# Kernel optimization log

Hardware: AMD Instinct MI355X
Metric: run time of the kernel (lower is better)

## Reference

```python
import jax, jax.numpy as jnp
import numpy as np

N_ENTITY = 30000
N_MOVIE = 6000
D = 384            # entity_hidden_size = hidden_size // 2
H = 768            # hidden_size
HT = 768           # token_hidden_size
N_LAYER = 12
N_BLOCK = 2
N_HEAD = 12
HEAD_DIM = H // N_HEAD
NUM_REL = 12
NUM_BASES = 8
E_KG = 200000
E_C = 200000
E_S = 80000
B = 16
LE = 48
LT = 256


def setup_inputs() -> dict:
    key = jax.random.key(0)
    ks = iter(jax.random.split(key, 48))
    nk = lambda: next(ks)
    rn = lambda shape, s=0.02: jax.random.normal(nk(), shape, dtype=jnp.float32) * s
    ri = lambda shape, m: jax.random.randint(nk(), shape, 0, m)
    return {
        'node_embeds': rn((N_ENTITY, D), 0.05),
        'rgcn_bases': rn((NUM_BASES, D, D)),
        'rgcn_comp': rn((NUM_REL, NUM_BASES), 0.3),
        'rgcn_root': rn((D, D)),
        'rgcn_bias': rn((D,), 0.01),
        'ep1_w1': rn((D, D // 2)), 'ep1_b1': rn((D // 2,), 0.01),
        'ep1_w2': rn((D // 2, D)), 'ep1_b2': rn((D,), 0.01),
        'ep2_w': rn((D, H)), 'ep2_b': rn((H,), 0.01),
        'tp1_w1': rn((HT, HT // 2)), 'tp1_b1': rn((HT // 2,), 0.01),
        'tp1_w2': rn((HT // 2, HT)), 'tp1_b2': rn((HT,), 0.01),
        'tp2_w': rn((HT, H)), 'tp2_b': rn((H,), 0.01),
        'ca_w': rn((H, H)),
        'pp1_w1': rn((H, H // 2)), 'pp1_b1': rn((H // 2,), 0.01),
        'pp1_w2': rn((H // 2, H)), 'pp1_b2': rn((H,), 0.01),
        'pp2_w': rn((H, N_LAYER * N_BLOCK * H)), 'pp2_b': rn((N_LAYER * N_BLOCK * H,), 0.01),
        'token_embeds': jax.random.normal(nk(), (B, LT, HT), dtype=jnp.float32),
        'edge_index': ri((2, E_KG), N_ENTITY),
        'edge_type': ri((E_KG,), NUM_REL),
        'edge_index_c': ri((2, E_C), N_ENTITY),
        'edge_index_t_s': ri((2, E_S), N_MOVIE),
        'edge_index_i_s': ri((2, E_S), N_MOVIE),
        'movie_to_entity': ri((N_MOVIE,), N_ENTITY),
        'entity_ids': ri((B, LE), N_ENTITY),
    }


def _mlp(x, w1, b1, w2, b2):
    return jax.nn.relu(x @ w1 + b1) @ w2 + b2


def _gcn(x, edge_index):
    # CustomGCNConv: add self loops, symmetric deg^{-1/2} norm, scatter-add
    n = x.shape[0]
    loop = jnp.arange(n)
    src = jnp.concatenate([edge_index[0], loop])
    dst = jnp.concatenate([edge_index[1], loop])
    deg = jax.ops.segment_sum(jnp.ones_like(dst, dtype=x.dtype), dst, num_segments=n)
    dis = deg ** -0.5  # deg >= 1 due to self loops
    norm = dis[src] * dis[dst]
    return jax.ops.segment_sum(norm[:, None] * x[src], dst, num_segments=n)


def _rgcn(x, edge_index, edge_type, bases, comp, root, bias):
    # PyG RGCNConv with basis decomposition, mean aggregation per relation
    n = x.shape[0]
    src, dst = edge_index[0], edge_index[1]
    W = jnp.einsum('rb,bio->rio', comp, bases)  # [R, D, D]
    out = x @ root + bias
    for r in range(NUM_REL):
        mask = (edge_type == r).astype(x.dtype)
        cnt = jax.ops.segment_sum(mask, dst, num_segments=n)
        norm = mask / jnp.maximum(cnt[dst], 1.0)
        h = x @ W[r]
        out = out + jax.ops.segment_sum(norm[:, None] * h[src], dst, num_segments=n)
    return out


def reference(node_embeds, rgcn_bases, rgcn_comp, rgcn_root, rgcn_bias,
              ep1_w1, ep1_b1, ep1_w2, ep1_b2, ep2_w, ep2_b,
              tp1_w1, tp1_b1, tp1_w2, tp1_b2, tp2_w, tp2_b,
              ca_w, pp1_w1, pp1_b1, pp1_w2, pp1_b2, pp2_w, pp2_b,
              token_embeds, edge_index, edge_type, edge_index_c,
              edge_index_t_s, edge_index_i_s, movie_to_entity, entity_ids):
    # ---- get_entity_embeds ----
    ent0 = _rgcn(node_embeds, edge_index, edge_type, rgcn_bases, rgcn_comp, rgcn_root, rgcn_bias) + node_embeds
    nf = ent0[movie_to_entity]  # sorted_indices == idx_to_id_tensor (keys are range(n_movie))
    ts1 = _gcn(nf, edge_index_t_s)
    ts2 = _gcn(ts1, edge_index_t_s)  # ts3 computed in original but unused -> skipped
    mt = (ts1 + ts2) * 0.5
    is1 = _gcn(nf, edge_index_i_s)
    is2 = _gcn(is1, edge_index_i_s)
    mi = (is1 + is2) * 0.5
    mm = (mt + mi) * 0.5
    c1 = _gcn(ent0, edge_index_c)
    c2 = _gcn(c1, edge_index_c)
    c3 = _gcn(c2, edge_index_c)
    ent = (c1 + c2 + c3 + ent0) * 0.25
    ent = ent.at[movie_to_entity].add(mm)  # index_add_
    ent = _mlp(ent, ep1_w1, ep1_b1, ep1_w2, ep1_b2) + ent
    ent = ent @ ep2_w + ep2_b  # [N_ENTITY, H]
    # ---- forward ----
    eemb = ent[entity_ids]  # [B, LE, H]
    tok = _mlp(token_embeds, tp1_w1, tp1_b1, tp1_w2, tp1_b2) + token_embeds
    tok = tok @ tp2_w + tp2_b  # [B, LT, H]
    attn = jnp.einsum('bth,beh->bte', tok @ ca_w, eemb) / H
    w = jax.nn.softmax(attn, axis=2)  # output_entity=False branch
    prompt = jnp.einsum('bte,beh->bth', w, eemb) + tok
    prompt = _mlp(prompt, pp1_w1, pp1_b1, pp1_w2, pp1_b2) + prompt
    prompt = prompt @ pp2_w + pp2_b  # [B, LT, N_LAYER*N_BLOCK*H]
    prompt = prompt.reshape(B, LT, N_LAYER, N_BLOCK, N_HEAD, HEAD_DIM)
    return prompt.transpose(2, 3, 0, 4, 1, 5)  # [n_layer, n_block, B, n_head, LT, head_dim]
```

## Files before the change

### kernel.cpp

```cpp
#include <hip/hip_runtime.h>
#include <hip/hip_bf16.h>
#include <cstdint>
#include <cstddef>


namespace {

constexpr int NE   = 30000;
constexpr int NM   = 6000;
constexpr int Dm   = 384;
constexpr int Hm   = 768;
constexpr int EKG  = 200000;
constexpr int EC   = 200000;
constexpr int ES   = 80000;
constexpr int Bc   = 16;
constexpr int LE   = 48;
constexpr int NTOK = 4096;
constexpr int NO   = 18432;

constexpr size_t NBf = (size_t)NE * Dm;
constexpr size_t MBF = (size_t)NM * Dm;

constexpr size_t P_XB    = 0;
constexpr size_t P_WCT   = 5760000;
constexpr size_t P_CNT   = 6644736;
constexpr size_t P_ENT0  = 7004736;
constexpr size_t P_HH    = 18524736;
constexpr size_t P_DIS   = 53084736;
constexpr size_t P_E0B   = 0;
constexpr size_t P_C1B   = 2880000;
constexpr size_t P_C2B   = 5760000;
constexpr size_t P_NFB   = 8640000;
constexpr size_t P_T1B   = 9800000;
constexpr size_t P_G1    = 11000000;
constexpr size_t P_ACC   = 41564736;
constexpr size_t P_ENTB  = 55600000;
constexpr size_t P_HIDB  = 0;
constexpr size_t P_ENT2B = 2880000;
constexpr size_t P_E768B = 8640000;
constexpr size_t P_TOKB  = 20160000;
constexpr size_t P_THIDB = 21732864;
constexpr size_t P_TOK1B = 22519296;
constexpr size_t P_TOK2B = 24092160;
constexpr size_t P_QB    = 25665024;
constexpr size_t P_EEMB  = 27237888;
constexpr size_t P_PR0   = 27532800;
constexpr size_t P_PR0B  = 30678528;
constexpr size_t P_PHIDB = 32251392;
constexpr size_t P_WT    = 74000000;
constexpr size_t S_ROOT  = 0;
constexpr size_t S_EP1A  = 147456;
constexpr size_t S_EP1B  = 221184;
constexpr size_t S_EP2   = 294912;
constexpr size_t S_TP1A  = 589824;
constexpr size_t S_TP1B  = 884736;
constexpr size_t S_TP2   = 1179648;
constexpr size_t S_CAW   = 1769472;
constexpr size_t S_PP1A  = 2359296;
constexpr size_t S_PP1B  = 2654208;

constexpr size_t WI       = 6291456 / 4;
constexpr size_t I_CNT    = WI + 0;
constexpr size_t I_PART   = WI + 30000;
constexpr size_t I_KG_RP  = WI + 30256;
constexpr size_t I_KG_CA  = WI + 60256;
constexpr size_t I_KG_SL  = WI + 90256;
constexpr size_t I_C_RP   = WI + 290256;
constexpr size_t I_C_CUR  = WI + 320256;
constexpr size_t I_C_SL   = WI + 350256;
constexpr size_t I_TS_RP  = WI + 550256;
constexpr size_t I_TS_CUR = WI + 556256;
constexpr size_t I_TS_SL  = WI + 562256;
constexpr size_t I_IS_RP  = WI + 642256;
constexpr size_t I_IS_CUR = WI + 648256;
constexpr size_t I_IS_SL  = WI + 654256;
constexpr size_t I_KG_BND = WI + 734256;
constexpr size_t I_KG_CB  = WI + 764256;
constexpr size_t WS_PP2T_BYTE = 6291456;
constexpr size_t WS_NEED      = 34603008;

inline int cdiv(long a, long b) { return (int)((a + b - 1) / b); }

}

typedef short short8v __attribute__((ext_vector_type(8)));
typedef float f32x4 __attribute__((ext_vector_type(4)));

__device__ __forceinline__ unsigned short f2bf(float f) {
  union { float f; uint32_t u; } v; v.f = f;
  uint32_t u = v.u;
  u += 0x7fffu + ((u >> 16) & 1u);
  return (unsigned short)(u >> 16);
}
__device__ __forceinline__ uint32_t pkbf(float a, float b) {
  __hip_bfloat162 h = __float22bfloat162_rn(float2{a, b});
  union { __hip_bfloat162 h; uint32_t u; } cv; cv.h = h;
  return cv.u;
}
__device__ __forceinline__ float bflo(uint32_t u) {
  union { uint32_t u; float f; } c; c.u = u << 16; return c.f;
}
__device__ __forceinline__ float bfhi(uint32_t u) {
  union { uint32_t u; float f; } c; c.u = u & 0xFFFF0000u; return c.f;
}

__device__ __forceinline__ void gl16(const void* g, void* l) {
  __builtin_amdgcn_global_load_lds(
      (const __attribute__((address_space(1))) void*)g,
      (__attribute__((address_space(3))) void*)l, 16, 0, 0);
}


__global__ void k_cvt(const float* __restrict__ x, unsigned short* __restrict__ o, size_t n2) {
  size_t i = (size_t)blockIdx.x * 256 + threadIdx.x;
  if (i >= n2) return;
  float2 v = *(const float2*)(x + 2 * i);
  *(uint32_t*)(o + 2 * i) = pkbf(v.x, v.y);
}

__global__ void k_cvt_t(const float* __restrict__ W, unsigned short* __restrict__ Wt,
                        int K, int N) {
  __shared__ float t[32][33];
  int tx = threadIdx.x & 31, ty = threadIdx.x >> 5;
  int n0 = blockIdx.x * 32, k0 = blockIdx.y * 32;
#pragma unroll
  for (int j = 0; j < 4; ++j)
    t[ty + 8 * j][tx] = W[(size_t)(k0 + ty + 8 * j) * N + n0 + tx];
  __syncthreads();
#pragma unroll
  for (int j = 0; j < 4; ++j) {
    int n = ty + 8 * j;
    Wt[(size_t)(n0 + n) * K + k0 + tx] = f2bf(t[tx][n]);
  }
}

__global__ void k_cvt_t_all(
    const float* s0, unsigned short* d0, const float* s1, unsigned short* d1,
    const float* s2, unsigned short* d2, const float* s3, unsigned short* d3,
    const float* s4, unsigned short* d4, const float* s5, unsigned short* d5,
    const float* s6, unsigned short* d6, const float* s7, unsigned short* d7,
    const float* s8, unsigned short* d8, const float* s9, unsigned short* d9) {
  __shared__ float t[32][33];
  int tile = blockIdx.x;
  const float* W; unsigned short* Wt; int K, N, base;
  if      (tile < 144)  { W = s0; Wt = d0; K = 384; N = 384; base = 0; }
  else if (tile < 216)  { W = s1; Wt = d1; K = 384; N = 192; base = 144; }
  else if (tile < 288)  { W = s2; Wt = d2; K = 192; N = 384; base = 216; }
  else if (tile < 576)  { W = s3; Wt = d3; K = 384; N = 768; base = 288; }
  else if (tile < 864)  { W = s4; Wt = d4; K = 768; N = 384; base = 576; }
  else if (tile < 1152) { W = s5; Wt = d5; K = 384; N = 768; base = 864; }
  else if (tile < 1728) { W = s6; Wt = d6; K = 768; N = 768; base = 1152; }
  else if (tile < 2304) { W = s7; Wt = d7; K = 768; N = 768; base = 1728; }
  else if (tile < 2592) { W = s8; Wt = d8; K = 768; N = 384; base = 2304; }
  else                  { W = s9; Wt = d9; K = 384; N = 768; base = 2592; }
  int lt = tile - base;
  int ntx = N >> 5;
  int n0 = (lt % ntx) * 32, k0 = (lt / ntx) * 32;
  int tx = threadIdx.x & 31, ty = threadIdx.x >> 5;
#pragma unroll
  for (int j = 0; j < 4; ++j)
    t[ty + 8 * j][tx] = W[(size_t)(k0 + ty + 8 * j) * N + n0 + tx];
  __syncthreads();
#pragma unroll
  for (int j = 0; j < 4; ++j) {
    int n = ty + 8 * j;
    Wt[(size_t)(n0 + n) * K + k0 + tx] = f2bf(t[tx][n]);
  }
}

__global__ void k_wcat(const float* __restrict__ comp, const float* __restrict__ bases,
                       unsigned short* __restrict__ Wt) {
  int idx = blockIdx.x * 256 + threadIdx.x;
  if (idx >= 12 * Dm * Dm) return;
  int i = idx % Dm;
  int o = (idx / Dm) % Dm;
  int r = idx / (Dm * Dm);
  float s = 0.f;
#pragma unroll
  for (int b = 0; b < 8; ++b)
    s += comp[r * 8 + b] * bases[(size_t)b * Dm * Dm + (size_t)i * Dm + o];
  Wt[idx] = f2bf(s);
}

__global__ void k_gather_b(const int* __restrict__ idx, const uint32_t* __restrict__ x2,
                           uint32_t* __restrict__ out2, int rows, int D2) {
  size_t i = (size_t)blockIdx.x * 256 + threadIdx.x;
  if (i >= (size_t)rows * D2) return;
  int r = (int)(i / D2);
  int c = (int)(i - (size_t)r * D2);
  out2[i] = x2[(size_t)idx[r] * D2 + c];
}

__global__ void k_scatter_movie(const int* __restrict__ mte, const float* __restrict__ g,
                                float* __restrict__ ent) {
  size_t i = (size_t)blockIdx.x * 256 + threadIdx.x;
  if (i >= MBF) return;
  int m = (int)(i / Dm);
  int d = (int)(i - (size_t)m * Dm);
  atomicAdd(&ent[(size_t)mte[m] * Dm + d], 0.25f * g[i]);
}


__global__ void k_hist(const int* __restrict__ dst, int* __restrict__ cnt, int E) {
  int e = blockIdx.x * 256 + threadIdx.x;
  if (e < E) atomicAdd(&cnt[dst[e]], 1);
}

__global__ void k_hist_lt(const int* __restrict__ dst, const int* __restrict__ typ,
                          int* __restrict__ cnt, int E) {
  int e = blockIdx.x * 256 + threadIdx.x;
  if (e < E && typ[e] < 6) atomicAdd(&cnt[dst[e]], 1);
}

__global__ void k_add_i(const int* __restrict__ a, const int* __restrict__ b,
                        int* __restrict__ o, int* __restrict__ o2, int n) {
  int i = blockIdx.x * 256 + threadIdx.x;
  if (i < n) { int v = a[i] + b[i]; o[i] = v; o2[i] = v; }
}

__global__ void k_scan_blk(const int* __restrict__ in, int* __restrict__ out,
                           int* __restrict__ part, int n) {
  __shared__ int s[256];
  int t = threadIdx.x;
  int g = blockIdx.x * 256 + t;
  int v = (g < n) ? in[g] : 0;
  s[t] = v;
  __syncthreads();
  for (int off = 1; off < 256; off <<= 1) {
    int add = (t >= off) ? s[t - off] : 0;
    __syncthreads();
    s[t] += add;
    __syncthreads();
  }
  if (g < n) out[g] = s[t] - v;
  if (t == 255) part[blockIdx.x] = s[255];
}

__global__ void k_scan_top(int* __restrict__ part, int nb) {
  __shared__ int s[256];
  int t = threadIdx.x;
  int v = (t < nb) ? part[t] : 0;
  s[t] = v;
  __syncthreads();
  for (int off = 1; off < 256; off <<= 1) {
    int add = (t >= off) ? s[t - off] : 0;
    __syncthreads();
    s[t] += add;
    __syncthreads();
  }
  if (t < nb) part[t] = s[t] - v;
}

__global__ void k_scan_add(int* __restrict__ out, const int* __restrict__ part,
                           int* __restrict__ cur, int n) {
  int g = blockIdx.x * 256 + threadIdx.x;
  if (g < n) { int v = out[g] + part[blockIdx.x]; out[g] = v; cur[g] = v; }
}

__global__ void k_fill(const int* __restrict__ src, const int* __restrict__ dst,
                       int* __restrict__ cur, int* __restrict__ slots, int E) {
  int e = blockIdx.x * 256 + threadIdx.x;
  if (e >= E) return;
  int d = dst[e];
  int pos = atomicAdd(&cur[d], 1);
  slots[pos] = src[e];
}

__global__ void k_fill_split(const int* __restrict__ src, const int* __restrict__ dst,
                             const int* __restrict__ typ, int* __restrict__ cur_a,
                             int* __restrict__ cur_b, int* __restrict__ slots, int E) {
  int e = blockIdx.x * 256 + threadIdx.x;
  if (e >= E) return;
  int d = dst[e];
  int* c = (typ[e] < 6) ? cur_a : cur_b;
  int pos = atomicAdd(&c[d], 1);
  slots[pos] = src[e] | (typ[e] << 16);
}

__global__ void k_dis_rp(const int* __restrict__ rp, float* __restrict__ dis, int n, int E) {
  int v = blockIdx.x * 256 + threadIdx.x;
  if (v >= n) return;
  int e0 = rp[v], e1 = (v + 1 < n) ? rp[v + 1] : E;
  dis[v] = rsqrtf((float)(e1 - e0) + 1.0f);
}

__global__ void k_count_type(const int* __restrict__ dst, const int* __restrict__ typ,
                             float* __restrict__ cnt, int E) {
  int i = blockIdx.x * 256 + threadIdx.x;
  if (i < E) atomicAdd(&cnt[(size_t)typ[i] * NE + dst[i]], 1.0f);
}

__global__ void k_rcp(float* __restrict__ c, size_t n) {
  size_t i = (size_t)blockIdx.x * 256 + threadIdx.x;
  if (i < n) { float v = c[i]; c[i] = (v > 0.f) ? 1.0f / v : 0.f; }
}

template <int OUTM, int ACCM>
__global__ void k_gcn_gb(const unsigned short* __restrict__ x,
                         const float* __restrict__ dis,
                         const int* __restrict__ rp, const int* __restrict__ slots,
                         unsigned short* __restrict__ outb, float* __restrict__ acc,
                         int n, int E, float sc) {
  int v = (int)((blockIdx.x * (size_t)blockDim.x + threadIdx.x) >> 6);
  int lane = threadIdx.x & 63;
  if (v >= n) return;
  float dv = dis[v];
  const uint32_t* xr = (const uint32_t*)(x + (size_t)v * Dm);
  float xv[6];
#pragma unroll
  for (int i = 0; i < 3; ++i) {
    uint32_t u = xr[lane + 64 * i];
    xv[2 * i] = bflo(u); xv[2 * i + 1] = bfhi(u);
  }
  float a[6];
#pragma unroll
  for (int i = 0; i < 6; ++i) a[i] = dv * xv[i];
  int e0 = rp[v], e1 = (v + 1 < n) ? rp[v + 1] : E;
  int e = e0;
  for (; e + 2 <= e1; e += 2) {
    int s0 = slots[e], s1 = slots[e + 1];
    float c0 = dis[s0], c1 = dis[s1];
    const uint32_t* x0 = (const uint32_t*)(x + (size_t)s0 * Dm);
    const uint32_t* x1 = (const uint32_t*)(x + (size_t)s1 * Dm);
    uint32_t u0[3], u1[3];
#pragma unroll
    for (int i = 0; i < 3; ++i) { u0[i] = x0[lane + 64 * i]; u1[i] = x1[lane + 64 * i]; }
#pragma unroll
    for (int i = 0; i < 3; ++i) {
      a[2 * i]     = fmaf(c0, bflo(u0[i]), a[2 * i]);
      a[2 * i + 1] = fmaf(c0, bfhi(u0[i]), a[2 * i + 1]);
      a[2 * i]     = fmaf(c1, bflo(u1[i]), a[2 * i]);
      a[2 * i + 1] = fmaf(c1, bfhi(u1[i]), a[2 * i + 1]);
    }
  }
  if (e < e1) {
    int s0 = slots[e];
    float c0 = dis[s0];
    const uint32_t* x0 = (const uint32_t*)(x + (size_t)s0 * Dm);
#pragma unroll
    for (int i = 0; i < 3; ++i) {
      uint32_t u = x0[lane + 64 * i];
      a[2 * i]     = fmaf(c0, bflo(u), a[2 * i]);
      a[2 * i + 1] = fmaf(c0, bfhi(u), a[2 * i + 1]);
    }
  }
#pragma unroll
  for (int i = 0; i < 6; ++i) a[i] *= dv;
  if (OUTM == 1) {
    uint32_t* ob = (uint32_t*)(outb + (size_t)v * Dm);
#pragma unroll
    for (int i = 0; i < 3; ++i) ob[lane + 64 * i] = pkbf(a[2 * i], a[2 * i + 1]);
  }
  float* ar = acc + (size_t)v * Dm;
  float nw[6];
#pragma unroll
  for (int i = 0; i < 3; ++i) {
    int cidx = 2 * (lane + 64 * i);
    if (ACCM == 1) {
      float2 old = *(const float2*)(ar + cidx);
      nw[2 * i] = old.x + sc * a[2 * i];
      nw[2 * i + 1] = old.y + sc * a[2 * i + 1];
    } else if (ACCM == 2) {
      nw[2 * i] = sc * (xv[2 * i] + a[2 * i]);
      nw[2 * i + 1] = sc * (xv[2 * i + 1] + a[2 * i + 1]);
    } else {
      nw[2 * i] = sc * a[2 * i];
      nw[2 * i + 1] = sc * a[2 * i + 1];
    }
    *(float2*)(ar + cidx) = float2{nw[2 * i], nw[2 * i + 1]};
  }
  if (OUTM == 2) {
    uint32_t* ob = (uint32_t*)(outb + (size_t)v * Dm);
#pragma unroll
    for (int i = 0; i < 3; ++i) ob[lane + 64 * i] = pkbf(nw[2 * i], nw[2 * i + 1]);
  }
}

template <bool FIRST, bool EMITB>
__global__ void k_rgcn_g(const unsigned short* __restrict__ hh, const float* __restrict__ rcp,
                         const int* __restrict__ rp, const int* __restrict__ bnd,
                         const int* __restrict__ slots, float* __restrict__ ent0,
                         unsigned short* __restrict__ outb, int E) {
  int v = (int)((blockIdx.x * (size_t)blockDim.x + threadIdx.x) >> 6);
  int lane = threadIdx.x & 63;
  if (v >= NE) return;
  const int rbase = FIRST ? 0 : 6;
  int e0, e1;
  if (FIRST) { e0 = rp[v]; e1 = bnd[v]; }
  else       { e0 = bnd[v]; e1 = (v + 1 < NE) ? rp[v + 1] : E; }
  float* er = ent0 + (size_t)v * Dm;
  float2 a[3];
#pragma unroll
  for (int i = 0; i < 3; ++i) a[i] = *(const float2*)(er + 2 * lane + 128 * i);
  int e = e0;
  for (; e + 2 <= e1; e += 2) {
    int p0 = slots[e], p1 = slots[e + 1];
    int r0 = (p0 >> 16) - rbase, s0 = p0 & 0xFFFF;
    int r1 = (p1 >> 16) - rbase, s1 = p1 & 0xFFFF;
    float nm0 = rcp[(size_t)(r0 + rbase) * NE + v];
    float nm1 = rcp[(size_t)(r1 + rbase) * NE + v];
    const uint32_t* h0 = (const uint32_t*)(hh + (size_t)s0 * 2304 + (size_t)r0 * 384);
    const uint32_t* h1 = (const uint32_t*)(hh + (size_t)s1 * 2304 + (size_t)r1 * 384);
    uint32_t u0[3], u1[3];
#pragma unroll
    for (int i = 0; i < 3; ++i) { u0[i] = h0[lane + 64 * i]; u1[i] = h1[lane + 64 * i]; }
#pragma unroll
    for (int i = 0; i < 3; ++i) {
      a[i].x = fmaf(nm0, bflo(u0[i]), a[i].x);
      a[i].y = fmaf(nm0, bfhi(u0[i]), a[i].y);
      a[i].x = fmaf(nm1, bflo(u1[i]), a[i].x);
      a[i].y = fmaf(nm1, bfhi(u1[i]), a[i].y);
    }
  }
  if (e < e1) {
    int p0 = slots[e];
    int r0 = (p0 >> 16) - rbase, s0 = p0 & 0xFFFF;
    float nm0 = rcp[(size_t)(r0 + rbase) * NE + v];
    const uint32_t* h0 = (const uint32_t*)(hh + (size_t)s0 * 2304 + (size_t)r0 * 384);
#pragma unroll
    for (int i = 0; i < 3; ++i) {
      uint32_t u = h0[lane + 64 * i];
      a[i].x = fmaf(nm0, bflo(u), a[i].x);
      a[i].y = fmaf(nm0, bfhi(u), a[i].y);
    }
  }
#pragma unroll
  for (int i = 0; i < 3; ++i) *(float2*)(er + 2 * lane + 128 * i) = a[i];
  if (EMITB) {
    uint32_t* ob = (uint32_t*)(outb + (size_t)v * Dm);
#pragma unroll
    for (int i = 0; i < 3; ++i) ob[lane + 64 * i] = pkbf(a[i].x, a[i].y);
  }
}

template <bool RELU, bool RES, int OUT, int SWZ>
__global__ __launch_bounds__(256) void mgemm_bf(
    const unsigned short* __restrict__ A, const unsigned short* __restrict__ Wt,
    const float* __restrict__ bias, const float* __restrict__ Rp,
    void* __restrict__ Cv, int M, int N, int K) {
  __shared__ __align__(16) unsigned short As[128 * 64];
  __shared__ __align__(16) unsigned short Bs[128 * 64];
  const int tid = threadIdx.x;
  const int lane = tid & 63;
  const int w = tid >> 6;
  int bm, bn;
  if (SWZ) {
    int bid = blockIdx.y * gridDim.x + blockIdx.x;
    int cpx = (gridDim.x * gridDim.y) >> 3;
    int swz = (bid & 7) * cpx + (bid >> 3);
    bm = (swz % gridDim.x) * 128;
    bn = (swz / gridDim.x) * 128;
  } else {
    bm = blockIdx.x * 128;
    bn = blockIdx.y * 128;
  }
  const int wr = (w >> 1) * 64, wc = (w & 1) * 64;
  const int lrow = lane & 15, lq = lane >> 4;
  f32x4 acc[4][4] = {};
  const int prow_l = lane >> 3;
  const int pslot = lane & 7;

  for (int k0 = 0; k0 < K; k0 += 64) {
    __syncthreads();
#pragma unroll
    for (int j = 0; j < 4; ++j) {
      int seg = j * 4 + w;
      int prow = seg * 8 + prow_l;
      int aslot = pslot ^ (prow & 7);
      int arow = min(bm + prow, M - 1);
      gl16(A + (size_t)arow * K + k0 + aslot * 8, &As[seg * 512 + lane * 8]);
    }
#pragma unroll
    for (int j = 0; j < 4; ++j) {
      int seg = j * 4 + w;
      int prow = seg * 8 + prow_l;
      int bslot = pslot ^ (prow & 7);
      int brow = min(bn + prow, N - 1);
      gl16(Wt + (size_t)brow * K + k0 + bslot * 8, &Bs[seg * 512 + lane * 8]);
    }
    __syncthreads();
#pragma unroll
    for (int ks = 0; ks < 2; ++ks) {
      short8v af[4], bf[4];
      const int slot = ks * 4 + lq;
#pragma unroll
      for (int mr = 0; mr < 4; ++mr) {
        int r = wr + mr * 16 + lrow;
        af[mr] = *(const short8v*)&As[r * 64 + ((slot ^ (r & 7)) << 3)];
      }
#pragma unroll
      for (int nc = 0; nc < 4; ++nc) {
        int r = wc + nc * 16 + lrow;
        bf[nc] = *(const short8v*)&Bs[r * 64 + ((slot ^ (r & 7)) << 3)];
      }
#pragma unroll
      for (int mr = 0; mr < 4; ++mr)
#pragma unroll
        for (int nc = 0; nc < 4; ++nc)
          acc[mr][nc] = __builtin_amdgcn_mfma_f32_16x16x32_bf16(
              af[mr], bf[nc], acc[mr][nc], 0, 0, 0);
    }
  }
  size_t colb[4];
  if (OUT == 2) {
#pragma unroll
    for (int nc = 0; nc < 4; ++nc) {
      int c = bn + wc + nc * 16 + lrow;
      int l = c / 1536, rem = c - l * 1536;
      int blk = rem / 768, rem2 = rem - blk * 768;
      int h2 = rem2 >> 6, dd = rem2 & 63;
      colb[nc] = (size_t)(l * 2 + blk) * 3145728 + (size_t)h2 * 16384 + dd;
    }
  }
#pragma unroll
  for (int mr = 0; mr < 4; ++mr) {
#pragma unroll
    for (int e = 0; e < 4; ++e) {
      int r = bm + wr + mr * 16 + lq * 4 + e;
      if (r >= M) continue;
      size_t rowoff = 0;
      if (OUT == 2) rowoff = (size_t)r * 64 + (size_t)(r >> 8) * 180224;
#pragma unroll
      for (int nc = 0; nc < 4; ++nc) {
        int c = bn + wc + nc * 16 + lrow;
        if (c >= N) continue;
        float v = acc[mr][nc][e];
        if (bias) v += bias[c];
        if (RES) v += Rp[(size_t)r * N + c];
        if (RELU) v = fmaxf(v, 0.f);
        if (OUT == 0) {
          ((float*)Cv)[(size_t)r * N + c] = v;
        } else if (OUT == 1) {
          ((unsigned short*)Cv)[(size_t)r * N + c] = f2bf(v);
        } else {
          ((float*)Cv)[colb[nc] + rowoff] = v;
        }
      }
    }
  }
}

__global__ __launch_bounds__(256) void mgemm_fin(
    const unsigned short* __restrict__ A, const float* __restrict__ W,
    const float* __restrict__ bias, float* __restrict__ O, int M, int N, int K) {
  __shared__ __align__(16) unsigned short As[128 * 64];
  __shared__ __align__(16) unsigned short Bs[128 * 64];
  const int tid = threadIdx.x;
  const int lane = tid & 63;
  const int w = tid >> 6;
  const int bm = blockIdx.x * 128, bn = blockIdx.y * 128;
  const int wr = (w >> 1) * 64, wc = (w & 1) * 64;
  const int lrow = lane & 15, lq = lane >> 4;
  f32x4 acc[4][4] = {};
  const int prow_l = lane >> 3;
  const int pslot = lane & 7;
  const int n_loc = tid & 127;
  const int kh = (tid >> 7) * 32;

  for (int k0 = 0; k0 < K; k0 += 64) {
    __syncthreads();
#pragma unroll
    for (int j = 0; j < 4; ++j) {
      int seg = j * 4 + w;
      int prow = seg * 8 + prow_l;
      int aslot = pslot ^ (prow & 7);
      gl16(A + (size_t)(bm + prow) * K + k0 + aslot * 8, &As[seg * 512 + lane * 8]);
    }
    float wv[32];
    const float* wp = W + (size_t)(k0 + kh) * N + bn + n_loc;
#pragma unroll
    for (int j = 0; j < 32; ++j) wv[j] = wp[(size_t)j * N];
#pragma unroll
    for (int c = 0; c < 4; ++c) {
      uint32_t u0 = pkbf(wv[8 * c + 0], wv[8 * c + 1]);
      uint32_t u1 = pkbf(wv[8 * c + 2], wv[8 * c + 3]);
      uint32_t u2 = pkbf(wv[8 * c + 4], wv[8 * c + 5]);
      uint32_t u3 = pkbf(wv[8 * c + 6], wv[8 * c + 7]);
      int s = (kh >> 3) + c;
      *(uint4*)&Bs[n_loc * 64 + ((s ^ (n_loc & 7)) << 3)] = uint4{u0, u1, u2, u3};
    }
    __syncthreads();
#pragma unroll
    for (int ks = 0; ks < 2; ++ks) {
      short8v af[4], bf[4];
      const int slot = ks * 4 + lq;
#pragma unroll
      for (int mr = 0; mr < 4; ++mr) {
        int r = wr + mr * 16 + lrow;
        af[mr] = *(const short8v*)&As[r * 64 + ((slot ^ (r & 7)) << 3)];
      }
#pragma unroll
      for (int nc = 0; nc < 4; ++nc) {
        int r = wc + nc * 16 + lrow;
        bf[nc] = *(const short8v*)&Bs[r * 64 + ((slot ^ (r & 7)) << 3)];
      }
#pragma unroll
      for (int mr = 0; mr < 4; ++mr)
#pragma unroll
        for (int nc = 0; nc < 4; ++nc)
          acc[mr][nc] = __builtin_amdgcn_mfma_f32_16x16x32_bf16(
              af[mr], bf[nc], acc[mr][nc], 0, 0, 0);
    }
  }
#pragma unroll
  for (int mr = 0; mr < 4; ++mr) {
#pragma unroll
    for (int e = 0; e < 4; ++e) {
      int r = bm + wr + mr * 16 + lq * 4 + e;
      int b = r >> 8, t = r & 255;
#pragma unroll
      for (int nc = 0; nc < 4; ++nc) {
        int c = bn + wc + nc * 16 + lrow;
        float v = acc[mr][nc][e] + bias[c];
        int l = c / 1536, rem = c - l * 1536;
        int blk = rem / 768, rem2 = rem - blk * 768;
        int hh = rem2 >> 6, dd = rem2 & 63;
        size_t oi = (((((size_t)l * 2 + blk) * 16 + b) * 12 + hh) * 256 + t) * 64 + dd;
        O[oi] = v;
      }
    }
  }
}

__global__ __launch_bounds__(256) void k_attn(
    const unsigned short* __restrict__ qb, const unsigned short* __restrict__ eb_all,
    const unsigned short* __restrict__ tokb, float* __restrict__ pr0,
    unsigned short* __restrict__ pr0b) {
  int gw = (int)((blockIdx.x * (size_t)blockDim.x + threadIdx.x) >> 6);
  int lane = threadIdx.x & 63;
  if (gw >= NTOK) return;
  int b = gw >> 8;
  const unsigned short* qr = qb + (size_t)gw * Hm;
  float2 q[6];
#pragma unroll
  for (int i = 0; i < 6; ++i) {
    uint32_t u = *(const uint32_t*)(qr + 2 * lane + 128 * i);
    q[i] = float2{bflo(u), bfhi(u)};
  }
  const unsigned short* eb = eb_all + (size_t)b * LE * Hm;
  float myA = -3.0e38f;
  for (int e = 0; e < LE; ++e) {
    const unsigned short* er = eb + (size_t)e * Hm;
    float s = 0.f;
#pragma unroll
    for (int i = 0; i < 6; ++i) {
      uint32_t u = *(const uint32_t*)(er + 2 * lane + 128 * i);
      s = fmaf(q[i].x, bflo(u), s);
      s = fmaf(q[i].y, bfhi(u), s);
    }
#pragma unroll
    for (int off = 32; off > 0; off >>= 1) s += __shfl_xor(s, off);
    if (lane == e) myA = s * (1.0f / 768.0f);
  }
  float mx = myA;
#pragma unroll
  for (int off = 32; off > 0; off >>= 1) mx = fmaxf(mx, __shfl_xor(mx, off));
  float p = (lane < LE) ? expf(myA - mx) : 0.f;
  float sum = p;
#pragma unroll
  for (int off = 32; off > 0; off >>= 1) sum += __shfl_xor(sum, off);
  float wgt = p / sum;
  const unsigned short* tr = tokb + (size_t)gw * Hm;
  float2 a[6];
#pragma unroll
  for (int i = 0; i < 6; ++i) {
    uint32_t u = *(const uint32_t*)(tr + 2 * lane + 128 * i);
    a[i] = float2{bflo(u), bfhi(u)};
  }
  for (int e = 0; e < LE; ++e) {
    float we = __shfl(wgt, e);
    const unsigned short* er = eb + (size_t)e * Hm;
#pragma unroll
    for (int i = 0; i < 6; ++i) {
      uint32_t u = *(const uint32_t*)(er + 2 * lane + 128 * i);
      a[i].x = fmaf(we, bflo(u), a[i].x);
      a[i].y = fmaf(we, bfhi(u), a[i].y);
    }
  }
  float* orow = pr0 + (size_t)gw * Hm;
  unsigned short* obrow = pr0b + (size_t)gw * Hm;
#pragma unroll
  for (int i = 0; i < 6; ++i) {
    *(float2*)(orow + 2 * lane + 128 * i) = a[i];
    *(uint32_t*)(obrow + 2 * lane + 128 * i) = pkbf(a[i].x, a[i].y);
  }
}


extern "C" void kernel_launch(void* const* d_in, const int* in_sizes, int n_in,
                              void* d_out, int out_size, void* d_ws, size_t ws_size,
                              hipStream_t stream) {
  (void)in_sizes; (void)n_in; (void)out_size;

  const float* x_node = (const float*)d_in[0];
  const float* bases  = (const float*)d_in[1];
  const float* comp   = (const float*)d_in[2];
  const float* root   = (const float*)d_in[3];
  const float* rbias  = (const float*)d_in[4];
  const float* ep1w1  = (const float*)d_in[5];
  const float* ep1b1  = (const float*)d_in[6];
  const float* ep1w2  = (const float*)d_in[7];
  const float* ep1b2  = (const float*)d_in[8];
  const float* ep2w   = (const float*)d_in[9];
  const float* ep2b   = (const float*)d_in[10];
  const float* tp1w1  = (const float*)d_in[11];
  const float* tp1b1  = (const float*)d_in[12];
  const float* tp1w2  = (const float*)d_in[13];
  const float* tp1b2  = (const float*)d_in[14];
  const float* tp2w   = (const float*)d_in[15];
  const float* tp2b   = (const float*)d_in[16];
  const float* caw    = (const float*)d_in[17];
  const float* pp1w1  = (const float*)d_in[18];
  const float* pp1b1  = (const float*)d_in[19];
  const float* pp1w2  = (const float*)d_in[20];
  const float* pp1b2  = (const float*)d_in[21];
  const float* pp2w   = (const float*)d_in[22];
  const float* pp2b   = (const float*)d_in[23];
  const float* tokens = (const float*)d_in[24];
  const int* ei_kg = (const int*)d_in[25];
  const int* etype = (const int*)d_in[26];
  const int* ei_c  = (const int*)d_in[27];
  const int* ei_ts = (const int*)d_in[28];
  const int* ei_is = (const int*)d_in[29];
  const int* mte   = (const int*)d_in[30];
  const int* eids  = (const int*)d_in[31];

  float* O = (float*)d_out;
  unsigned short* xb    = (unsigned short*)(O + P_XB);
  unsigned short* wct   = (unsigned short*)(O + P_WCT);
  float* rcpc  = O + P_CNT;
  float* ent0  = O + P_ENT0;
  unsigned short* hh    = (unsigned short*)(O + P_HH);
  float* disc  = O + P_DIS;
  float* dist  = O + P_DIS + 30000;
  float* disi  = O + P_DIS + 36000;
  unsigned short* ent0b = (unsigned short*)(O + P_E0B);
  unsigned short* c1b   = (unsigned short*)(O + P_C1B);
  unsigned short* c2b   = (unsigned short*)(O + P_C2B);
  unsigned short* nfb   = (unsigned short*)(O + P_NFB);
  unsigned short* t1b   = (unsigned short*)(O + P_T1B);
  float* g1    = O + P_G1;
  float* accb  = O + P_ACC;
  unsigned short* entb  = (unsigned short*)(O + P_ENTB);
  unsigned short* hidb  = (unsigned short*)(O + P_HIDB);
  unsigned short* ent2b = (unsigned short*)(O + P_ENT2B);
  unsigned short* e768b = (unsigned short*)(O + P_E768B);
  unsigned short* tokb  = (unsigned short*)(O + P_TOKB);
  unsigned short* thidb = (unsigned short*)(O + P_THIDB);
  unsigned short* tok1b = (unsigned short*)(O + P_TOK1B);
  unsigned short* tok2b = (unsigned short*)(O + P_TOK2B);
  unsigned short* qb    = (unsigned short*)(O + P_QB);
  unsigned short* eemb  = (unsigned short*)(O + P_EEMB);
  float* pr0   = O + P_PR0;
  unsigned short* pr0b  = (unsigned short*)(O + P_PR0B);
  unsigned short* phidb = (unsigned short*)(O + P_PHIDB);
  unsigned short* wts   = (unsigned short*)(O + P_WT);

  int* iws = (int*)d_ws;
  unsigned short* p2b = (unsigned short*)d_ws;
  unsigned short* pp2t = (unsigned short*)d_ws + WS_PP2T_BYTE / 2;
  const bool ws_ok = (ws_size >= WS_NEED);
  int* cnt_i  = iws + I_CNT;
  int* part   = iws + I_PART;
  int* kg_rp  = iws + I_KG_RP;  int* kg_ca = iws + I_KG_CA;  int* kg_sl = iws + I_KG_SL;
  int* kg_bnd = iws + I_KG_BND; int* kg_cb = iws + I_KG_CB;
  int* c_rp   = iws + I_C_RP;   int* c_cur  = iws + I_C_CUR;   int* c_sl  = iws + I_C_SL;
  int* ts_rp  = iws + I_TS_RP;  int* ts_cur = iws + I_TS_CUR;  int* ts_sl = iws + I_TS_SL;
  int* is_rp  = iws + I_IS_RP;  int* is_cur = iws + I_IS_CUR;  int* is_sl = iws + I_IS_SL;

  const int EW = 256;

  k_cvt<<<cdiv(NBf / 2, EW), EW, 0, stream>>>(x_node, xb, NBf / 2);
  k_wcat<<<cdiv(12 * Dm * Dm, EW), EW, 0, stream>>>(comp, bases, wct);
  k_cvt_t_all<<<2880, 256, 0, stream>>>(
      root, wts + S_ROOT, ep1w1, wts + S_EP1A, ep1w2, wts + S_EP1B,
      ep2w, wts + S_EP2, tp1w1, wts + S_TP1A, tp1w2, wts + S_TP1B,
      tp2w, wts + S_TP2, caw, wts + S_CAW, pp1w1, wts + S_PP1A,
      pp1w2, wts + S_PP1B);

  hipMemsetAsync(cnt_i, 0, (size_t)NE * 4, stream);
  k_hist<<<cdiv(EKG, EW), EW, 0, stream>>>(ei_kg + EKG, cnt_i, EKG);
  {
    int nb = cdiv(NE, 256);
    k_scan_blk<<<nb, 256, 0, stream>>>(cnt_i, kg_rp, part, NE);
    k_scan_top<<<1, 256, 0, stream>>>(part, nb);
    k_scan_add<<<nb, 256, 0, stream>>>(kg_rp, part, kg_ca, NE);
  }
  hipMemsetAsync(cnt_i, 0, (size_t)NE * 4, stream);
  k_hist_lt<<<cdiv(EKG, EW), EW, 0, stream>>>(ei_kg + EKG, etype, cnt_i, EKG);
  k_add_i<<<cdiv(NE, EW), EW, 0, stream>>>(kg_rp, cnt_i, kg_bnd, kg_cb, NE);
  k_fill_split<<<cdiv(EKG, EW), EW, 0, stream>>>(
      ei_kg, ei_kg + EKG, etype, kg_ca, kg_cb, kg_sl, EKG);

  auto build_csr = [&](const int* ei, int n, int E, int* rp, int* cur, int* sl) {
    hipMemsetAsync(cnt_i, 0, (size_t)n * 4, stream);
    k_hist<<<cdiv(E, EW), EW, 0, stream>>>(ei + E, cnt_i, E);
    int nb = cdiv(n, 256);
    k_scan_blk<<<nb, 256, 0, stream>>>(cnt_i, rp, part, n);
    k_scan_top<<<1, 256, 0, stream>>>(part, nb);
    k_scan_add<<<nb, 256, 0, stream>>>(rp, part, cur, n);
    k_fill<<<cdiv(E, EW), EW, 0, stream>>>(ei, ei + E, cur, sl, E);
  };
  build_csr(ei_c, NE, EC, c_rp, c_cur, c_sl);
  build_csr(ei_ts, NM, ES, ts_rp, ts_cur, ts_sl);
  build_csr(ei_is, NM, ES, is_rp, is_cur, is_sl);

  k_dis_rp<<<cdiv(NE, EW), EW, 0, stream>>>(c_rp, disc, NE, EC);
  k_dis_rp<<<cdiv(NM, EW), EW, 0, stream>>>(ts_rp, dist, NM, ES);
  k_dis_rp<<<cdiv(NM, EW), EW, 0, stream>>>(is_rp, disi, NM, ES);

  hipMemsetAsync(rcpc, 0, (size_t)12 * NE * 4, stream);
  k_count_type<<<cdiv(EKG, EW), EW, 0, stream>>>(ei_kg + EKG, etype, rcpc, EKG);
  k_rcp<<<cdiv((long)12 * NE, EW), EW, 0, stream>>>(rcpc, (size_t)12 * NE);

  mgemm_bf<false, true, 0, 0><<<dim3(cdiv(NE, 128), cdiv(Dm, 128)), 256, 0, stream>>>(
      xb, wts + S_ROOT, rbias, x_node, ent0, NE, Dm, Dm);
  mgemm_bf<false, false, 1, 0><<<dim3(cdiv(NE, 128), cdiv(6 * Dm, 128)), 256, 0, stream>>>(
      xb, wct, nullptr, nullptr, hh, NE, 6 * Dm, Dm);
  k_rgcn_g<true, false><<<cdiv((long)NE * 64, EW), EW, 0, stream>>>(
      hh, rcpc, kg_rp, kg_bnd, kg_sl, ent0, nullptr, EKG);
  mgemm_bf<false, false, 1, 0><<<dim3(cdiv(NE, 128), cdiv(6 * Dm, 128)), 256, 0, stream>>>(
      xb, wct + (size_t)6 * Dm * Dm, nullptr, nullptr, hh, NE, 6 * Dm, Dm);
  k_rgcn_g<false, true><<<cdiv((long)NE * 64, EW), EW, 0, stream>>>(
      hh, rcpc, kg_rp, kg_bnd, kg_sl, ent0, ent0b, EKG);

  k_gather_b<<<cdiv((long)NM * 192, EW), EW, 0, stream>>>(
      mte, (const uint32_t*)ent0b, (uint32_t*)nfb, NM, 192);
  k_gcn_gb<1, 3><<<cdiv((long)NM * 64, EW), EW, 0, stream>>>(
      nfb, dist, ts_rp, ts_sl, t1b, g1, NM, ES, 1.0f);
  k_gcn_gb<0, 1><<<cdiv((long)NM * 64, EW), EW, 0, stream>>>(
      t1b, dist, ts_rp, ts_sl, nullptr, g1, NM, ES, 1.0f);
  k_gcn_gb<1, 1><<<cdiv((long)NM * 64, EW), EW, 0, stream>>>(
      nfb, disi, is_rp, is_sl, t1b, g1, NM, ES, 1.0f);
  k_gcn_gb<0, 1><<<cdiv((long)NM * 64, EW), EW, 0, stream>>>(
      t1b, disi, is_rp, is_sl, nullptr, g1, NM, ES, 1.0f);
  k_gcn_gb<1, 2><<<cdiv((long)NE * 64, EW), EW, 0, stream>>>(
      ent0b, disc, c_rp, c_sl, c1b, accb, NE, EC, 0.25f);
  k_gcn_gb<1, 1><<<cdiv((long)NE * 64, EW), EW, 0, stream>>>(
      c1b, disc, c_rp, c_sl, c2b, accb, NE, EC, 0.25f);
  k_scatter_movie<<<cdiv(MBF, EW), EW, 0, stream>>>(mte, g1, accb);
  k_gcn_gb<2, 1><<<cdiv((long)NE * 64, EW), EW, 0, stream>>>(
      c2b, disc, c_rp, c_sl, entb, accb, NE, EC, 0.25f);

  if (ws_ok) {
    k_cvt_t<<<dim3(NO / 32, Hm / 32), 256, 0, stream>>>(pp2w, pp2t, Hm, NO);
  }

  mgemm_bf<true, false, 1, 0><<<dim3(cdiv(NE, 128), cdiv(192, 128)), 256, 0, stream>>>(
      entb, wts + S_EP1A, ep1b1, nullptr, hidb, NE, 192, Dm);
  mgemm_bf<false, true, 1, 0><<<dim3(cdiv(NE, 128), cdiv(Dm, 128)), 256, 0, stream>>>(
      hidb, wts + S_EP1B, ep1b2, accb, ent2b, NE, Dm, 192);
  mgemm_bf<false, false, 1, 0><<<dim3(cdiv(NE, 128), cdiv(Hm, 128)), 256, 0, stream>>>(
      ent2b, wts + S_EP2, ep2b, nullptr, e768b, NE, Hm, Dm);

  k_cvt<<<cdiv((long)NTOK * Hm / 2, EW), EW, 0, stream>>>(tokens, tokb, (size_t)NTOK * Hm / 2);
  mgemm_bf<true, false, 1, 0><<<dim3(cdiv(NTOK, 128), cdiv(Dm, 128)), 256, 0, stream>>>(
      tokb, wts + S_TP1A, tp1b1, nullptr, thidb, NTOK, Dm, Hm);
  mgemm_bf<false, true, 1, 0><<<dim3(cdiv(NTOK, 128), cdiv(Hm, 128)), 256, 0, stream>>>(
      thidb, wts + S_TP1B, tp1b2, tokens, tok1b, NTOK, Hm, Dm);
  mgemm_bf<false, false, 1, 0><<<dim3(cdiv(NTOK, 128), cdiv(Hm, 128)), 256, 0, stream>>>(
      tok1b, wts + S_TP2, tp2b, nullptr, tok2b, NTOK, Hm, Hm);
  mgemm_bf<false, false, 1, 0><<<dim3(cdiv(NTOK, 128), cdiv(Hm, 128)), 256, 0, stream>>>(
      tok2b, wts + S_CAW, nullptr, nullptr, qb, NTOK, Hm, Hm);

  k_gather_b<<<cdiv((long)Bc * LE * (Hm / 2), EW), EW, 0, stream>>>(
      eids, (const uint32_t*)e768b, (uint32_t*)eemb, Bc * LE, Hm / 2);
  k_attn<<<cdiv((long)NTOK * 64, 256), 256, 0, stream>>>(qb, eemb, tok2b, pr0, pr0b);

  mgemm_bf<true, false, 1, 0><<<dim3(cdiv(NTOK, 128), cdiv(Dm, 128)), 256, 0, stream>>>(
      pr0b, wts + S_PP1A, pp1b1, nullptr, phidb, NTOK, Dm, Hm);
  mgemm_bf<false, true, 1, 0><<<dim3(cdiv(NTOK, 128), cdiv(Hm, 128)), 256, 0, stream>>>(
      phidb, wts + S_PP1B, pp1b2, pr0, p2b, NTOK, Hm, Dm);

  if (ws_ok) {
    mgemm_bf<false, false, 2, 1><<<dim3(NTOK / 128, NO / 128), 256, 0, stream>>>(
        p2b, pp2t, pp2b, nullptr, O, NTOK, NO, Hm);
  } else {
    mgemm_fin<<<dim3(NTOK / 128, NO / 128), 256, 0, stream>>>(
        p2b, pp2w, pp2b, O, NTOK, NO, Hm);
  }
}
```

Measured before the change: 1.555 ms.

## Batch independent GCN propagations into combined launches and drop GEMM block swizzle

Merges the first-hop GCN passes over the co-occurrence graph and the two movie graphs into one launch, and likewise the second hops, by splitting block ranges across the three graphs. The two movie paths now get separate scratch buffers (t2b, g2), and a combined scatter adds both into the entity accumulator. This removes several small serialized launches and lets the movie-graph work fill the GPU alongside the larger entity-graph work. Separately, the L2-oriented block swizzle in the final large GEMM is removed, which may change cache reuse for that output projection.

```diff
diff --git a/kernel.cpp b/kernel.cpp
--- a/kernel.cpp
+++ b/kernel.cpp
@@ -28,11 +28,13 @@
 constexpr size_t P_HH    = 18524736;
 constexpr size_t P_DIS   = 53084736;
 constexpr size_t P_E0B   = 0;
-constexpr size_t P_C1B   = 2880000;
-constexpr size_t P_C2B   = 5760000;
-constexpr size_t P_NFB   = 8640000;
-constexpr size_t P_T1B   = 9800000;
-constexpr size_t P_G1    = 11000000;
+constexpr size_t P_C1B   = 7004736;
+constexpr size_t P_C2B   = 12764736;
+constexpr size_t P_NFB   = 18600000;
+constexpr size_t P_T1B   = 19800000;
+constexpr size_t P_G1    = 21000000;
+constexpr size_t P_T2B   = 23400000;
+constexpr size_t P_G2    = 24600000;
 constexpr size_t P_ACC   = 41564736;
 constexpr size_t P_ENTB  = 55600000;
 constexpr size_t P_HIDB  = 0;
@@ -79,6 +81,9 @@
 constexpr size_t WS_PP2T_BYTE = 6291456;
 constexpr size_t WS_NEED      = 34603008;
 
+constexpr int NBLK_E = (NE * 64) / 256;
+constexpr int NBLK_M = (NM * 64) / 256;
+
 inline int cdiv(long a, long b) { return (int)((a + b - 1) / b); }
 
 }
@@ -191,13 +196,13 @@
   out2[i] = x2[(size_t)idx[r] * D2 + c];
 }
 
-__global__ void k_scatter_movie(const int* __restrict__ mte, const float* __restrict__ g,
-                                float* __restrict__ ent) {
+__global__ void k_scatter_movie2(const int* __restrict__ mte, const float* __restrict__ g1,
+                                 const float* __restrict__ g2, float* __restrict__ ent) {
   size_t i = (size_t)blockIdx.x * 256 + threadIdx.x;
   if (i >= MBF) return;
   int m = (int)(i / Dm);
   int d = (int)(i - (size_t)m * Dm);
-  atomicAdd(&ent[(size_t)mte[m] * Dm + d], 0.25f * g[i]);
+  atomicAdd(&ent[(size_t)mte[m] * Dm + d], 0.25f * (g1[i] + g2[i]));
 }
 
 
@@ -296,12 +301,12 @@
 }
 
 template <int OUTM, int ACCM>
-__global__ void k_gcn_gb(const unsigned short* __restrict__ x,
-                         const float* __restrict__ dis,
-                         const int* __restrict__ rp, const int* __restrict__ slots,
-                         unsigned short* __restrict__ outb, float* __restrict__ acc,
-                         int n, int E, float sc) {
-  int v = (int)((blockIdx.x * (size_t)blockDim.x + threadIdx.x) >> 6);
+__device__ __forceinline__ void gcn_body(
+    const unsigned short* __restrict__ x, const float* __restrict__ dis,
+    const int* __restrict__ rp, const int* __restrict__ slots,
+    unsigned short* __restrict__ outb, float* __restrict__ acc,
+    int n, int E, float sc, int blk) {
+  int v = (int)(((size_t)blk * 256 + threadIdx.x) >> 6);
   int lane = threadIdx.x & 63;
   if (v >= n) return;
   float dv = dis[v];
@@ -373,6 +378,49 @@
     uint32_t* ob = (uint32_t*)(outb + (size_t)v * Dm);
 #pragma unroll
     for (int i = 0; i < 3; ++i) ob[lane + 64 * i] = pkbf(nw[2 * i], nw[2 * i + 1]);
+  }
+}
+
+template <int OUTM, int ACCM>
+__global__ void k_gcn_gb(const unsigned short* __restrict__ x, const float* __restrict__ dis,
+                         const int* __restrict__ rp, const int* __restrict__ slots,
+                         unsigned short* __restrict__ outb, float* __restrict__ acc,
+                         int n, int E, float sc) {
+  gcn_body<OUTM, ACCM>(x, dis, rp, slots, outb, acc, n, E, sc, blockIdx.x);
+}
+
+__global__ void k_gcn_r1(const unsigned short* e0b, const float* disc,
+                         const int* c_rp, const int* c_sl,
+                         unsigned short* c1b, float* accb,
+                         const unsigned short* nfb,
+                         const float* dist, const int* ts_rp, const int* ts_sl,
+                         unsigned short* t1b, float* g1,
+                         const float* disi, const int* is_rp, const int* is_sl,
+                         unsigned short* t2b, float* g2) {
+  int blk = blockIdx.x;
+  if (blk < NBLK_E) {
+    gcn_body<1, 2>(e0b, disc, c_rp, c_sl, c1b, accb, NE, EC, 0.25f, blk);
+  } else if (blk < NBLK_E + NBLK_M) {
+    gcn_body<1, 3>(nfb, dist, ts_rp, ts_sl, t1b, g1, NM, ES, 1.0f, blk - NBLK_E);
+  } else {
+    gcn_body<1, 3>(nfb, disi, is_rp, is_sl, t2b, g2, NM, ES, 1.0f, blk - NBLK_E - NBLK_M);
+  }
+}
+
+__global__ void k_gcn_r2(const unsigned short* c1b, const float* disc,
+                         const int* c_rp, const int* c_sl,
+                         unsigned short* c2b, float* accb,
+                         const unsigned short* t1b,
+                         const float* dist, const int* ts_rp, const int* ts_sl, float* g1,
+                         const unsigned short* t2b,
+                         const float* disi, const int* is_rp, const int* is_sl, float* g2) {
+  int blk = blockIdx.x;
+  if (blk < NBLK_E) {
+    gcn_body<1, 1>(c1b, disc, c_rp, c_sl, c2b, accb, NE, EC, 0.25f, blk);
+  } else if (blk < NBLK_E + NBLK_M) {
+    gcn_body<0, 1>(t1b, dist, ts_rp, ts_sl, nullptr, g1, NM, ES, 1.0f, blk - NBLK_E);
+  } else {
+    gcn_body<0, 1>(t2b, disi, is_rp, is_sl, nullptr, g2, NM, ES, 1.0f, blk - NBLK_E - NBLK_M);
   }
 }
 
@@ -433,7 +481,7 @@
   }
 }
 
-template <bool RELU, bool RES, int OUT, int SWZ>
+template <bool RELU, bool RES, int OUT>
 __global__ __launch_bounds__(256) void mgemm_bf(
     const unsigned short* __restrict__ A, const unsigned short* __restrict__ Wt,
     const float* __restrict__ bias, const float* __restrict__ Rp,
@@ -443,17 +491,7 @@
   const int tid = threadIdx.x;
   const int lane = tid & 63;
   const int w = tid >> 6;
-  int bm, bn;
-  if (SWZ) {
-    int bid = blockIdx.y * gridDim.x + blockIdx.x;
-    int cpx = (gridDim.x * gridDim.y) >> 3;
-    int swz = (bid & 7) * cpx + (bid >> 3);
-    bm = (swz % gridDim.x) * 128;
-    bn = (swz / gridDim.x) * 128;
-  } else {
-    bm = blockIdx.x * 128;
-    bn = blockIdx.y * 128;
-  }
+  const int bm = blockIdx.x * 128, bn = blockIdx.y * 128;
   const int wr = (w >> 1) * 64, wc = (w & 1) * 64;
   const int lrow = lane & 15, lq = lane >> 4;
   f32x4 acc[4][4] = {};
@@ -739,7 +777,9 @@
   unsigned short* c2b   = (unsigned short*)(O + P_C2B);
   unsigned short* nfb   = (unsigned short*)(O + P_NFB);
   unsigned short* t1b   = (unsigned short*)(O + P_T1B);
+  unsigned short* t2b   = (unsigned short*)(O + P_T2B);
   float* g1    = O + P_G1;
+  float* g2    = O + P_G2;
   float* accb  = O + P_ACC;
   unsigned short* entb  = (unsigned short*)(O + P_ENTB);
   unsigned short* hidb  = (unsigned short*)(O + P_HIDB);
@@ -813,67 +853,63 @@
   k_count_type<<<cdiv(EKG, EW), EW, 0, stream>>>(ei_kg + EKG, etype, rcpc, EKG);
   k_rcp<<<cdiv((long)12 * NE, EW), EW, 0, stream>>>(rcpc, (size_t)12 * NE);
 
-  mgemm_bf<false, true, 0, 0><<<dim3(cdiv(NE, 128), cdiv(Dm, 128)), 256, 0, stream>>>(
+  mgemm_bf<false, true, 0><<<dim3(cdiv(NE, 128), cdiv(Dm, 128)), 256, 0, stream>>>(
       xb, wts + S_ROOT, rbias, x_node, ent0, NE, Dm, Dm);
-  mgemm_bf<false, false, 1, 0><<<dim3(cdiv(NE, 128), cdiv(6 * Dm, 128)), 256, 0, stream>>>(
+  mgemm_bf<false, false, 1><<<dim3(cdiv(NE, 128), cdiv(6 * Dm, 128)), 256, 0, stream>>>(
       xb, wct, nullptr, nullptr, hh, NE, 6 * Dm, Dm);
   k_rgcn_g<true, false><<<cdiv((long)NE * 64, EW), EW, 0, stream>>>(
       hh, rcpc, kg_rp, kg_bnd, kg_sl, ent0, nullptr, EKG);
-  mgemm_bf<false, false, 1, 0><<<dim3(cdiv(NE, 128), cdiv(6 * Dm, 128)), 256, 0, stream>>>(
+  mgemm_bf<false, false, 1><<<dim3(cdiv(NE, 128), cdiv(6 * Dm, 128)), 256, 0, stream>>>(
       xb, wct + (size_t)6 * Dm * Dm, nullptr, nullptr, hh, NE, 6 * Dm, Dm);
   k_rgcn_g<false, true><<<cdiv((long)NE * 64, EW), EW, 0, stream>>>(
       hh, rcpc, kg_rp, kg_bnd, kg_sl, ent0, ent0b, EKG);
 
   k_gather_b<<<cdiv((long)NM * 192, EW), EW, 0, stream>>>(
       mte, (const uint32_t*)ent0b, (uint32_t*)nfb, NM, 192);
-  k_gcn_gb<1, 3><<<cdiv((long)NM * 64, EW), EW, 0, stream>>>(
-      nfb, dist, ts_rp, ts_sl, t1b, g1, NM, ES, 1.0f);
-  k_gcn_gb<0, 1><<<cdiv((long)NM * 64, EW), EW, 0, stream>>>(
-      t1b, dist, ts_rp, ts_sl, nullptr, g1, NM, ES, 1.0f);
-  k_gcn_gb<1, 1><<<cdiv((long)NM * 64, EW), EW, 0, stream>>>(
-      nfb, disi, is_rp, is_sl, t1b, g1, NM, ES, 1.0f);
-  k_gcn_gb<0, 1><<<cdiv((long)NM * 64, EW), EW, 0, stream>>>(
-      t1b, disi, is_rp, is_sl, nullptr, g1, NM, ES, 1.0f);
-  k_gcn_gb<1, 2><<<cdiv((long)NE * 64, EW), EW, 0, stream>>>(
-      ent0b, disc, c_rp, c_sl, c1b, accb, NE, EC, 0.25f);
-  k_gcn_gb<1, 1><<<cdiv((long)NE * 64, EW), EW, 0, stream>>>(
-      c1b, disc, c_rp, c_sl, c2b, accb, NE, EC, 0.25f);
-  k_scatter_movie<<<cdiv(MBF, EW), EW, 0, stream>>>(mte, g1, accb);
-  k_gcn_gb<2, 1><<<cdiv((long)NE * 64, EW), EW, 0, stream>>>(
+  k_gcn_r1<<<NBLK_E + 2 * NBLK_M, 256, 0, stream>>>(
+      ent0b, disc, c_rp, c_sl, c1b, accb,
+      nfb, dist, ts_rp, ts_sl, t1b, g1,
+      disi, is_rp, is_sl, t2b, g2);
+  k_gcn_r2<<<NBLK_E + 2 * NBLK_M, 256, 0, stream>>>(
+      c1b, disc, c_rp, c_sl, c2b, accb,
+      t1b, dist, ts_rp, ts_sl, g1,
+      t2b, disi, is_rp, is_sl, g2);
+  k_scatter_movie2<<<cdiv(MBF, EW), EW, 0, stream>>>(mte, g1, g2, accb);
+  k_gcn_gb<2, 1><<<NBLK_E, 256, 0, stream>>>(
       c2b, disc, c_rp, c_sl, entb, accb, NE, EC, 0.25f);
 
   if (ws_ok) {
     k_cvt_t<<<dim3(NO / 32, Hm / 32), 256, 0, stream>>>(pp2w, pp2t, Hm, NO);
   }
 
-  mgemm_bf<true, false, 1, 0><<<dim3(cdiv(NE, 128), cdiv(192, 128)), 256, 0, stream>>>(
+  mgemm_bf<true, false, 1><<<dim3(cdiv(NE, 128), cdiv(192, 128)), 256, 0, stream>>>(
       entb, wts + S_EP1A, ep1b1, nullptr, hidb, NE, 192, Dm);
-  mgemm_bf<false, true, 1, 0><<<dim3(cdiv(NE, 128), cdiv(Dm, 128)), 256, 0, stream>>>(
+  mgemm_bf<false, true, 1><<<dim3(cdiv(NE, 128), cdiv(Dm, 128)), 256, 0, stream>>>(
       hidb, wts + S_EP1B, ep1b2, accb, ent2b, NE, Dm, 192);
-  mgemm_bf<false, false, 1, 0><<<dim3(cdiv(NE, 128), cdiv(Hm, 128)), 256, 0, stream>>>(
+  mgemm_bf<false, false, 1><<<dim3(cdiv(NE, 128), cdiv(Hm, 128)), 256, 0, stream>>>(
       ent2b, wts + S_EP2, ep2b, nullptr, e768b, NE, Hm, Dm);
 
   k_cvt<<<cdiv((long)NTOK * Hm / 2, EW), EW, 0, stream>>>(tokens, tokb, (size_t)NTOK * Hm / 2);
-  mgemm_bf<true, false, 1, 0><<<dim3(cdiv(NTOK, 128), cdiv(Dm, 128)), 256, 0, stream>>>(
+  mgemm_bf<true, false, 1><<<dim3(cdiv(NTOK, 128), cdiv(Dm, 128)), 256, 0, stream>>>(
       tokb, wts + S_TP1A, tp1b1, nullptr, thidb, NTOK, Dm, Hm);
-  mgemm_bf<false, true, 1, 0><<<dim3(cdiv(NTOK, 128), cdiv(Hm, 128)), 256, 0, stream>>>(
+  mgemm_bf<false, true, 1><<<dim3(cdiv(NTOK, 128), cdiv(Hm, 128)), 256, 0, stream>>>(
       thidb, wts + S_TP1B, tp1b2, tokens, tok1b, NTOK, Hm, Dm);
-  mgemm_bf<false, false, 1, 0><<<dim3(cdiv(NTOK, 128), cdiv(Hm, 128)), 256, 0, stream>>>(
+  mgemm_bf<false, false, 1><<<dim3(cdiv(NTOK, 128), cdiv(Hm, 128)), 256, 0, stream>>>(
       tok1b, wts + S_TP2, tp2b, nullptr, tok2b, NTOK, Hm, Hm);
-  mgemm_bf<false, false, 1, 0><<<dim3(cdiv(NTOK, 128), cdiv(Hm, 128)), 256, 0, stream>>>(
+  mgemm_bf<false, false, 1><<<dim3(cdiv(NTOK, 128), cdiv(Hm, 128)), 256, 0, stream>>>(
       tok2b, wts + S_CAW, nullptr, nullptr, qb, NTOK, Hm, Hm);
 
   k_gather_b<<<cdiv((long)Bc * LE * (Hm / 2), EW), EW, 0, stream>>>(
       eids, (const uint32_t*)e768b, (uint32_t*)eemb, Bc * LE, Hm / 2);
   k_attn<<<cdiv((long)NTOK * 64, 256), 256, 0, stream>>>(qb, eemb, tok2b, pr0, pr0b);
 
-  mgemm_bf<true, false, 1, 0><<<dim3(cdiv(NTOK, 128), cdiv(Dm, 128)), 256, 0, stream>>>(
+  mgemm_bf<true, false, 1><<<dim3(cdiv(NTOK, 128), cdiv(Dm, 128)), 256, 0, stream>>>(
       pr0b, wts + S_PP1A, pp1b1, nullptr, phidb, NTOK, Dm, Hm);
-  mgemm_bf<false, true, 1, 0><<<dim3(cdiv(NTOK, 128), cdiv(Hm, 128)), 256, 0, stream>>>(
+  mgemm_bf<false, true, 1><<<dim3(cdiv(NTOK, 128), cdiv(Hm, 128)), 256, 0, stream>>>(
       phidb, wts + S_PP1B, pp1b2, pr0, p2b, NTOK, Hm, Dm);
 
   if (ws_ok) {
-    mgemm_bf<false, false, 2, 1><<<dim3(NTOK / 128, NO / 128), 256, 0, stream>>>(
+    mgemm_bf<false, false, 2><<<dim3(NTOK / 128, NO / 128), 256, 0, stream>>>(
         p2b, pp2t, pp2b, nullptr, O, NTOK, NO, Hm);
   } else {
     mgemm_fin<<<dim3(NTOK / 128, NO / 128), 256, 0, stream>>>(
```

New measurement: 1.518 ms. 2.4% less time.
